# Performance work log

Measured on AMD Instinct MI355X. Metric: run time of the kernel, lower is better.

The kernel has to match this reference:

```python
import jax, jax.numpy as jnp
import numpy as np

DRUG_DIM, PROT_DIM, HIDDEN_DIM, OUTPUT_DIM = 128, 128, 256, 256


def setup_inputs() -> dict:
    key = jax.random.key(0)
    ks = jax.random.split(key, 7)
    B, n_d, n_p = 8, 64, 1024
    s = lambda d: 1.0 / np.sqrt(d)
    return {
        "X_d": jax.random.normal(ks[0], (B, n_d, DRUG_DIM), dtype=jnp.float32),
        "X_p": jax.random.normal(ks[1], (B, n_p, PROT_DIM), dtype=jnp.float32),
        # nn.Linear(in, out) weights have shape (out, in); we store transposed (in, out)
        "W_d": jax.random.uniform(ks[2], (DRUG_DIM, HIDDEN_DIM), jnp.float32, -s(DRUG_DIM), s(DRUG_DIM)),
        "W_p": jax.random.uniform(ks[3], (PROT_DIM, HIDDEN_DIM), jnp.float32, -s(PROT_DIM), s(PROT_DIM)),
        "W_a": jax.random.uniform(ks[4], (DRUG_DIM, OUTPUT_DIM), jnp.float32, -s(DRUG_DIM), s(DRUG_DIM)),
        "W_b": jax.random.uniform(ks[5], (PROT_DIM, OUTPUT_DIM), jnp.float32, -s(PROT_DIM), s(PROT_DIM)),
        "w_score": jax.random.uniform(ks[6], (HIDDEN_DIM,), jnp.float32, -s(HIDDEN_DIM), s(HIDDEN_DIM)),
    }


def reference(X_d, X_p, W_d, W_p, W_a, W_b, w_score):
    # Projections: (B, n_d, H), (B, n_p, H), (B, n_d, O), (B, n_p, O)
    hd = jnp.einsum("bik,kh->bih", X_d, W_d)
    hp = jnp.einsum("bjk,kh->bjh", X_p, W_p)
    fd = jnp.einsum("bik,ko->bio", X_d, W_a)
    fp = jnp.einsum("bjk,ko->bjo", X_p, W_b)

    # N_ij = tanh(hd_i + hp_j): (B, n_d, n_p, H); scores = N @ w_score
    N = jnp.tanh(hd[:, :, None, :] + hp[:, None, :, :])
    scores = jnp.einsum("bijh,h->bij", N, w_score)
    A = jax.nn.softmax(scores, axis=-1)  # softmax over protein dim

    # f_ij = tanh(fd_i + fp_j): (B, n_d, n_p, O)
    f = jnp.tanh(fd[:, :, None, :] + fp[:, None, :, :])
    X_int = jnp.einsum("bij,bijo->bo", A, f)  # sum over i and j
    return X_int
```

## Files before the change

kernel.cpp:

```cpp
#include <hip/hip_runtime.h>

#define NB   8
#define ND   64
#define NP   1024
#define KDIM 128
#define HID  256
#define OUTD 256
#define CSC  2.885390081777927f
#define PSTR 520

typedef __attribute__((ext_vector_type(8))) short  bf16x8;
typedef __attribute__((ext_vector_type(4))) float  f32x4;


__device__ __forceinline__ ushort f2bf(float f) {
    unsigned u = __float_as_uint(f);
    return (ushort)((u + 0x7FFFu + ((u >> 16) & 1u)) >> 16);
}

__global__ __launch_bounds__(256) void k_cast(
    const float* __restrict__ Xd, const float* __restrict__ Xp,
    const float* __restrict__ Wd, const float* __restrict__ Wa,
    const float* __restrict__ Wp, const float* __restrict__ Wb,
    ushort* __restrict__ Xdbf, ushort* __restrict__ Xpbf,
    ushort* __restrict__ WdT, ushort* __restrict__ WaT,
    ushort* __restrict__ WpT, ushort* __restrict__ WbT) {
    int blk = blockIdx.x, t = threadIdx.x;
    if (blk < 1024) {
        size_t i = ((size_t)blk << 10) + ((size_t)t << 2);
        float4 v = *(const float4*)(Xp + i);
        ushort4 o; o.x = f2bf(v.x); o.y = f2bf(v.y); o.z = f2bf(v.z); o.w = f2bf(v.w);
        *(ushort4*)(Xpbf + i) = o;
    } else if (blk < 1088) {
        size_t i = ((size_t)(blk - 1024) << 10) + ((size_t)t << 2);
        float4 v = *(const float4*)(Xd + i);
        ushort4 o; o.x = f2bf(v.x); o.y = f2bf(v.y); o.z = f2bf(v.z); o.w = f2bf(v.w);
        *(ushort4*)(Xdbf + i) = o;
    } else {
        int r = blk - 1088, mat = r >> 5;
        const float* W = (mat == 0) ? Wd : (mat == 1) ? Wa : (mat == 2) ? Wp : Wb;
        ushort* WT = (mat == 0) ? WdT : (mat == 1) ? WaT : (mat == 2) ? WpT : WbT;
        int o0 = ((r & 31) << 10) + (t << 2);
        int n = o0 >> 7, k0 = o0 & 127;
        ushort4 o;
        o.x = f2bf(W[(k0 + 0) * HID + n]);
        o.y = f2bf(W[(k0 + 1) * HID + n]);
        o.z = f2bf(W[(k0 + 2) * HID + n]);
        o.w = f2bf(W[(k0 + 3) * HID + n]);
        *(ushort4*)(WT + o0) = o;
    }
}

__global__ __launch_bounds__(256) void k_proj_mfma(
    const ushort* __restrict__ Xpbf, const ushort* __restrict__ Xdbf,
    const ushort* __restrict__ WdT, const ushort* __restrict__ WaT,
    const ushort* __restrict__ WpT, const ushort* __restrict__ WbT,
    float* __restrict__ Ehd, float* __restrict__ Efd,
    float* __restrict__ EhpT, float* __restrict__ Efp) {
    int blk = blockIdx.x, t = threadIdx.x;
    const ushort *A, *B;
    float* out; size_t obase; int ostride, am0, bn0;
    if (blk < 512) {
        int mt = blk >> 2, nt = blk & 3;
        A = Xpbf; am0 = mt * 64; B = WbT; bn0 = nt * 64;
        out = Efp; obase = (size_t)am0 * HID + bn0; ostride = HID;
    } else if (blk < 1024) {
        int r = blk - 512, b = r >> 6, rr = r & 63;
        int mt = rr >> 4, nt = rr & 15;
        A = WpT; am0 = mt * 64;
        B = Xpbf + (size_t)b * NP * KDIM; bn0 = nt * 64;
        out = EhpT; obase = ((size_t)(b * 256 + am0)) * NP + bn0; ostride = NP;
    } else if (blk < 1056) {
        int r = blk - 1024; int mt = r >> 2, nt = r & 3;
        A = Xdbf; am0 = mt * 64; B = WdT; bn0 = nt * 64;
        out = Ehd; obase = (size_t)am0 * HID + bn0; ostride = HID;
    } else {
        int r = blk - 1056; int mt = r >> 2, nt = r & 3;
        A = Xdbf; am0 = mt * 64; B = WaT; bn0 = nt * 64;
        out = Efd; obase = (size_t)am0 * HID + bn0; ostride = HID;
    }
    int l = t & 63, w = t >> 6;
    int wm = (w >> 1) << 5, wn = (w & 1) << 5;
    int lr = l & 15, lk = (l >> 4) << 3;
    const ushort* Ab = A + (size_t)(am0 + wm + lr) * KDIM + lk;
    const ushort* Bb = B + (size_t)(bn0 + wn + lr) * KDIM + lk;

    bf16x8 af[2][4], bfr[2][4];
#pragma unroll
    for (int f = 0; f < 2; ++f)
#pragma unroll
        for (int ks = 0; ks < 4; ++ks) {
            af[f][ks]  = *(const bf16x8*)(Ab + (size_t)(f << 4) * KDIM + (ks << 5));
            bfr[f][ks] = *(const bf16x8*)(Bb + (size_t)(f << 4) * KDIM + (ks << 5));
        }

    f32x4 acc[2][2];
#pragma unroll
    for (int mf = 0; mf < 2; ++mf)
#pragma unroll
        for (int nf = 0; nf < 2; ++nf) acc[mf][nf] = (f32x4){0.f, 0.f, 0.f, 0.f};
#pragma unroll
    for (int ks = 0; ks < 4; ++ks)
#pragma unroll
        for (int mf = 0; mf < 2; ++mf)
#pragma unroll
            for (int nf = 0; nf < 2; ++nf)
                acc[mf][nf] = __builtin_amdgcn_mfma_f32_16x16x32_bf16(
                    af[mf][ks], bfr[nf][ks], acc[mf][nf], 0, 0, 0);

#pragma unroll
    for (int mf = 0; mf < 2; ++mf)
#pragma unroll
        for (int nf = 0; nf < 2; ++nf)
#pragma unroll
            for (int r = 0; r < 4; ++r) {
                int m = wm + (mf << 4) + ((l >> 4) << 2) + r;
                int n = wn + (nf << 4) + (l & 15);
                out[obase + (size_t)m * ostride + n] =
                    __builtin_amdgcn_exp2f(acc[mf][nf][r] * CSC);
            }
}

__global__ __launch_bounds__(512, 8) void k_fused(
    const float* __restrict__ Ehd, const float* __restrict__ EhpT,
    const float* __restrict__ Efd, const float* __restrict__ Efp,
    const float* __restrict__ wsc, float* __restrict__ num,
    float* __restrict__ den) {
    int blk = blockIdx.x;
    int b = blk & 7, pair = (blk >> 3) & 31, jh = blk >> 8;
    int row0 = b * ND + pair * 2;
    int t = threadIdx.x;

    __shared__ float2 hrow[256];
    __shared__ float  w2s[256];
    __shared__ float2 a2[256];
    __shared__ float  sred[8 * PSTR];
    __shared__ float  wsum0[4], wsum1[4];

    if (t < 256) {
        hrow[t] = make_float2(Ehd[((size_t)row0 << 8) + t],
                              Ehd[((size_t)(row0 + 1) << 8) + t]);
        w2s[t] = -2.0f * wsc[t];
    }
    __syncthreads();

    {
        int jq = t & 63, hq = t >> 6;
        const float* pB = EhpT + ((size_t)((b << 8) + (hq << 5))) * NP
                        + (jh << 8) + (jq << 2);
        float a00 = 0, a01 = 0, a02 = 0, a03 = 0;
        float a10 = 0, a11 = 0, a12 = 0, a13 = 0;
        for (int hh = 0; hh < 32; ++hh) {
            int h = (hq << 5) + hh;
            float2 hv = hrow[h];
            float wv = w2s[h];
            float4 p = *(const float4*)(pB + (size_t)hh * NP);
            a00 = fmaf(wv, __builtin_amdgcn_rcpf(fmaf(hv.x, p.x, 1.f)), a00);
            a01 = fmaf(wv, __builtin_amdgcn_rcpf(fmaf(hv.x, p.y, 1.f)), a01);
            a02 = fmaf(wv, __builtin_amdgcn_rcpf(fmaf(hv.x, p.z, 1.f)), a02);
            a03 = fmaf(wv, __builtin_amdgcn_rcpf(fmaf(hv.x, p.w, 1.f)), a03);
            a10 = fmaf(wv, __builtin_amdgcn_rcpf(fmaf(hv.y, p.x, 1.f)), a10);
            a11 = fmaf(wv, __builtin_amdgcn_rcpf(fmaf(hv.y, p.y, 1.f)), a11);
            a12 = fmaf(wv, __builtin_amdgcn_rcpf(fmaf(hv.y, p.z, 1.f)), a12);
            a13 = fmaf(wv, __builtin_amdgcn_rcpf(fmaf(hv.y, p.w, 1.f)), a13);
        }
        int base = (hq << 6) + jq;
        sred[0 * PSTR + base] = a00;  sred[1 * PSTR + base] = a01;
        sred[2 * PSTR + base] = a02;  sred[3 * PSTR + base] = a03;
        sred[4 * PSTR + base] = a10;  sred[5 * PSTR + base] = a11;
        sred[6 * PSTR + base] = a12;  sred[7 * PSTR + base] = a13;
    }
    __syncthreads();

    if (t < 256) {
        int jq2 = t >> 2, joff = t & 3;
        const float* p0 = sred + joff * PSTR + jq2;
        const float* p1 = sred + (4 + joff) * PSTR + jq2;
        float sc0 = 0.f, sc1 = 0.f;
#pragma unroll
        for (int hq = 0; hq < 8; ++hq) {
            sc0 += p0[hq << 6];
            sc1 += p1[hq << 6];
        }
        const float L2E = 1.4426950408889634f;
        float u0 = __builtin_amdgcn_exp2f(sc0 * L2E);
        float u1 = __builtin_amdgcn_exp2f(sc1 * L2E);
        a2[t] = make_float2(-2.f * u0, -2.f * u1);
        float s0 = u0, s1 = u1;
#pragma unroll
        for (int off = 32; off > 0; off >>= 1) {
            s0 += __shfl_xor(s0, off, 64);
            s1 += __shfl_xor(s1, off, 64);
        }
        if ((t & 63) == 0) { wsum0[t >> 6] = s0; wsum1[t >> 6] = s1; }
    }
    __syncthreads();
    if (t == 0) {
        den[((size_t)row0 << 2) + jh] =
            (wsum0[0] + wsum0[1]) + (wsum0[2] + wsum0[3]);
        den[((size_t)(row0 + 1) << 2) + jh] =
            (wsum1[0] + wsum1[1]) + (wsum1[2] + wsum1[3]);
    }

    {
        int oq = t & 63, jg = t >> 6;
        int o0 = oq << 2;
        float4 fd0 = *(const float4*)(Efd + ((size_t)row0 << 8) + o0);
        float4 fd1 = *(const float4*)(Efd + ((size_t)(row0 + 1) << 8) + o0);
        const float* fpB = Efp + ((size_t)(b * NP + (jh << 8) + (jg << 5)) << 8) + o0;
        float b00 = 0, b01 = 0, b02 = 0, b03 = 0;
        float b10 = 0, b11 = 0, b12 = 0, b13 = 0;
        for (int jj = 0; jj < 32; ++jj) {
            float4 f = *(const float4*)(fpB + ((size_t)jj << 8));
            float2 av = a2[(jg << 5) + jj];
            b00 = fmaf(av.x, __builtin_amdgcn_rcpf(fmaf(fd0.x, f.x, 1.f)), b00);
            b01 = fmaf(av.x, __builtin_amdgcn_rcpf(fmaf(fd0.y, f.y, 1.f)), b01);
            b02 = fmaf(av.x, __builtin_amdgcn_rcpf(fmaf(fd0.z, f.z, 1.f)), b02);
            b03 = fmaf(av.x, __builtin_amdgcn_rcpf(fmaf(fd0.w, f.w, 1.f)), b03);
            b10 = fmaf(av.y, __builtin_amdgcn_rcpf(fmaf(fd1.x, f.x, 1.f)), b10);
            b11 = fmaf(av.y, __builtin_amdgcn_rcpf(fmaf(fd1.y, f.y, 1.f)), b11);
            b12 = fmaf(av.y, __builtin_amdgcn_rcpf(fmaf(fd1.z, f.z, 1.f)), b12);
            b13 = fmaf(av.y, __builtin_amdgcn_rcpf(fmaf(fd1.w, f.w, 1.f)), b13);
        }
        __syncthreads();
        int base = (jg << 6) + oq;
        sred[0 * PSTR + base] = b00;  sred[1 * PSTR + base] = b01;
        sred[2 * PSTR + base] = b02;  sred[3 * PSTR + base] = b03;
        sred[4 * PSTR + base] = b10;  sred[5 * PSTR + base] = b11;
        sred[6 * PSTR + base] = b12;  sred[7 * PSTR + base] = b13;
    }
    __syncthreads();

    {
        int r = t >> 8, o = t & 255;
        const float* pk = sred + ((r << 2) + (o & 3)) * PSTR + (o >> 2);
        float s = 0.f;
#pragma unroll
        for (int g = 0; g < 8; ++g) s += pk[g << 6];
        num[(((size_t)(row0 + r) << 2) + jh) * 256 + o] = s;
    }
}

__global__ __launch_bounds__(256) void k_reduce(
    const float* __restrict__ num, const float* __restrict__ den,
    float* __restrict__ out) {
    int b = blockIdx.x, t = threadIdx.x;
    float s = 64.0f;
    for (int i = 0; i < 64; ++i) {
        size_t row = (size_t)(b * 64 + i);
        float D = (den[(row << 2) + 0] + den[(row << 2) + 1]) +
                  (den[(row << 2) + 2] + den[(row << 2) + 3]);
        const float* nb = num + (row << 2) * 256 + t;
        float n = (nb[0] + nb[256]) + (nb[512] + nb[768]);
        s += n * __builtin_amdgcn_rcpf(D);
    }
    out[(b << 8) + t] = s;
}

extern "C" void kernel_launch(void* const* d_in, const int* in_sizes, int n_in,
                              void* d_out, int out_size, void* d_ws, size_t ws_size,
                              hipStream_t stream) {
    const float* Xd  = (const float*)d_in[0];
    const float* Xp  = (const float*)d_in[1];
    const float* Wd  = (const float*)d_in[2];
    const float* Wp  = (const float*)d_in[3];
    const float* Wa  = (const float*)d_in[4];
    const float* Wb  = (const float*)d_in[5];
    const float* wsc = (const float*)d_in[6];
    float* out = (float*)d_out;

    float* ws = (float*)d_ws;
    float* Ehd  = ws;
    float* Efd  = Ehd + NB * ND * HID;
    float* EhpT = Efd + NB * ND * OUTD;
    float* Efp  = EhpT + NB * NP * HID;
    float* stage = Efp + NB * NP * OUTD;
    ushort* Xpbf = (ushort*)stage;
    ushort* Xdbf = Xpbf + NB * NP * KDIM;
    ushort* WdT  = Xdbf + 65536;
    ushort* WaT  = WdT + 32768;
    ushort* WpT  = WaT + 32768;
    ushort* WbT  = WpT + 32768;
    float* numb = stage + 622592;
    float* denb = numb + 524288;

    k_cast     <<<1216, 256, 0, stream>>>(Xd, Xp, Wd, Wa, Wp, Wb,
                                          Xdbf, Xpbf, WdT, WaT, WpT, WbT);
    k_proj_mfma<<<1088, 256, 0, stream>>>(Xpbf, Xdbf, WdT, WaT, WpT, WbT,
                                          Ehd, Efd, EhpT, Efp);
    k_fused    <<<1024, 512, 0, stream>>>(Ehd, EhpT, Efd, Efp, wsc, numb, denb);
    k_reduce   <<<NB, 256, 0, stream>>>(numb, denb, out);
}
```

Baseline: 64.96 us.

## Merge four reciprocals into one and process four drug rows per block

The fused attention kernel now combines four weighted reciprocal terms, sum c_i/u_i, into a single rational expression. This needs one rcp per four terms instead of four, cutting transcendental-unit work in both the score and output loops. Each block also handles four drug rows instead of two, so every loaded protein vector is reused across more rows and the grid is halved. In exchange, register and LDS use grow (launch bounds relaxed to 4 waves per SIMD), and the product of four denominators may overflow or underflow for extreme values, which affects accuracy.

```diff
diff --git a/kernel.cpp b/kernel.cpp
--- a/kernel.cpp
+++ b/kernel.cpp
@@ -8,6 +8,7 @@
 #define OUTD 256
 #define CSC  2.885390081777927f
 #define PSTR 520
+#define AST  264
 
 typedef __attribute__((ext_vector_type(8))) short  bf16x8;
 typedef __attribute__((ext_vector_type(4))) float  f32x4;
@@ -16,6 +17,17 @@
 __device__ __forceinline__ ushort f2bf(float f) {
     unsigned u = __float_as_uint(f);
     return (ushort)((u + 0x7FFFu + ((u >> 16) & 1u)) >> 16);
+}
+
+__device__ __forceinline__ float comb4(float u1, float u2, float u3, float u4,
+                                       float c1, float c2, float c3, float c4,
+                                       float acc) {
+    float p12 = u1 * u2, p34 = u3 * u4;
+    float P   = p12 * p34;
+    float t1  = fmaf(c1, u2, c2 * u1);
+    float t2  = fmaf(c3, u4, c4 * u3);
+    float num = fmaf(t1, p34, t2 * p12);
+    return fmaf(num, __builtin_amdgcn_rcpf(P), acc);
 }
 
 __global__ __launch_bounds__(256) void k_cast(
@@ -121,25 +133,27 @@
             }
 }
 
-__global__ __launch_bounds__(512, 8) void k_fused(
+__global__ __launch_bounds__(512, 4) void k_fused(
     const float* __restrict__ Ehd, const float* __restrict__ EhpT,
     const float* __restrict__ Efd, const float* __restrict__ Efp,
     const float* __restrict__ wsc, float* __restrict__ num,
     float* __restrict__ den) {
     int blk = blockIdx.x;
-    int b = blk & 7, pair = (blk >> 3) & 31, jh = blk >> 8;
-    int row0 = b * ND + pair * 2;
+    int b = blk & 7, quad = (blk >> 3) & 15, jo = blk >> 7;
+    int row0 = b * ND + quad * 4;
     int t = threadIdx.x;
 
-    __shared__ float2 hrow[256];
+    __shared__ float4 hrow4[256];
     __shared__ float  w2s[256];
-    __shared__ float2 a2[256];
-    __shared__ float  sred[8 * PSTR];
-    __shared__ float  wsum0[4], wsum1[4];
+    __shared__ float  a2s[4 * AST];
+    __shared__ float  sred[16 * PSTR];
+    __shared__ float  wsA[8], wsB[8];
 
     if (t < 256) {
-        hrow[t] = make_float2(Ehd[((size_t)row0 << 8) + t],
-                              Ehd[((size_t)(row0 + 1) << 8) + t]);
+        hrow4[t] = make_float4(Ehd[((size_t)row0 << 8) + t],
+                               Ehd[((size_t)(row0 + 1) << 8) + t],
+                               Ehd[((size_t)(row0 + 2) << 8) + t],
+                               Ehd[((size_t)(row0 + 3) << 8) + t]);
         w2s[t] = -2.0f * wsc[t];
     }
     __syncthreads();
@@ -147,59 +161,82 @@
     {
         int jq = t & 63, hq = t >> 6;
         const float* pB = EhpT + ((size_t)((b << 8) + (hq << 5))) * NP
-                        + (jh << 8) + (jq << 2);
-        float a00 = 0, a01 = 0, a02 = 0, a03 = 0;
-        float a10 = 0, a11 = 0, a12 = 0, a13 = 0;
-        for (int hh = 0; hh < 32; ++hh) {
-            int h = (hq << 5) + hh;
-            float2 hv = hrow[h];
-            float wv = w2s[h];
-            float4 p = *(const float4*)(pB + (size_t)hh * NP);
-            a00 = fmaf(wv, __builtin_amdgcn_rcpf(fmaf(hv.x, p.x, 1.f)), a00);
-            a01 = fmaf(wv, __builtin_amdgcn_rcpf(fmaf(hv.x, p.y, 1.f)), a01);
-            a02 = fmaf(wv, __builtin_amdgcn_rcpf(fmaf(hv.x, p.z, 1.f)), a02);
-            a03 = fmaf(wv, __builtin_amdgcn_rcpf(fmaf(hv.x, p.w, 1.f)), a03);
-            a10 = fmaf(wv, __builtin_amdgcn_rcpf(fmaf(hv.y, p.x, 1.f)), a10);
-            a11 = fmaf(wv, __builtin_amdgcn_rcpf(fmaf(hv.y, p.y, 1.f)), a11);
-            a12 = fmaf(wv, __builtin_amdgcn_rcpf(fmaf(hv.y, p.z, 1.f)), a12);
-            a13 = fmaf(wv, __builtin_amdgcn_rcpf(fmaf(hv.y, p.w, 1.f)), a13);
+                        + (jo << 8) + (jq << 2);
+        float acc[4][4];
+#pragma unroll
+        for (int r = 0; r < 4; ++r)
+#pragma unroll
+            for (int c = 0; c < 4; ++c) acc[r][c] = 0.f;
+        for (int hg = 0; hg < 8; ++hg) {
+            const float* pr = pB + (size_t)(hg << 2) * NP;
+            float4 p0 = *(const float4*)(pr);
+            float4 p1 = *(const float4*)(pr + NP);
+            float4 p2 = *(const float4*)(pr + 2 * (size_t)NP);
+            float4 p3 = *(const float4*)(pr + 3 * (size_t)NP);
+            int h = (hq << 5) + (hg << 2);
+            float4 h0 = hrow4[h],     h1 = hrow4[h + 1];
+            float4 h2 = hrow4[h + 2], h3 = hrow4[h + 3];
+            float w0 = w2s[h],     w1 = w2s[h + 1];
+            float w2 = w2s[h + 2], w3 = w2s[h + 3];
+#define ROW1(HC, AR)                                                          \
+            AR[0] = comb4(fmaf(h0.HC, p0.x, 1.f), fmaf(h1.HC, p1.x, 1.f),     \
+                          fmaf(h2.HC, p2.x, 1.f), fmaf(h3.HC, p3.x, 1.f),     \
+                          w0, w1, w2, w3, AR[0]);                             \
+            AR[1] = comb4(fmaf(h0.HC, p0.y, 1.f), fmaf(h1.HC, p1.y, 1.f),     \
+                          fmaf(h2.HC, p2.y, 1.f), fmaf(h3.HC, p3.y, 1.f),     \
+                          w0, w1, w2, w3, AR[1]);                             \
+            AR[2] = comb4(fmaf(h0.HC, p0.z, 1.f), fmaf(h1.HC, p1.z, 1.f),     \
+                          fmaf(h2.HC, p2.z, 1.f), fmaf(h3.HC, p3.z, 1.f),     \
+                          w0, w1, w2, w3, AR[2]);                             \
+            AR[3] = comb4(fmaf(h0.HC, p0.w, 1.f), fmaf(h1.HC, p1.w, 1.f),     \
+                          fmaf(h2.HC, p2.w, 1.f), fmaf(h3.HC, p3.w, 1.f),     \
+                          w0, w1, w2, w3, AR[3])
+            ROW1(x, acc[0]);
+            ROW1(y, acc[1]);
+            ROW1(z, acc[2]);
+            ROW1(w, acc[3]);
+#undef ROW1
         }
         int base = (hq << 6) + jq;
-        sred[0 * PSTR + base] = a00;  sred[1 * PSTR + base] = a01;
-        sred[2 * PSTR + base] = a02;  sred[3 * PSTR + base] = a03;
-        sred[4 * PSTR + base] = a10;  sred[5 * PSTR + base] = a11;
-        sred[6 * PSTR + base] = a12;  sred[7 * PSTR + base] = a13;
+#pragma unroll
+        for (int r = 0; r < 4; ++r)
+#pragma unroll
+            for (int c = 0; c < 4; ++c)
+                sred[((r << 2) + c) * PSTR + base] = acc[r][c];
     }
     __syncthreads();
 
-    if (t < 256) {
-        int jq2 = t >> 2, joff = t & 3;
-        const float* p0 = sred + joff * PSTR + jq2;
-        const float* p1 = sred + (4 + joff) * PSTR + jq2;
-        float sc0 = 0.f, sc1 = 0.f;
+    {
+        int j = t & 255, rh = t >> 8;
+        int jq2 = j >> 2, jc = j & 3;
+        int rA = rh << 1, rB = rA + 1;
+        const float* pA = sred + ((rA << 2) + jc) * PSTR + jq2;
+        const float* pB2 = sred + ((rB << 2) + jc) * PSTR + jq2;
+        float sA = 0.f, sB = 0.f;
 #pragma unroll
         for (int hq = 0; hq < 8; ++hq) {
-            sc0 += p0[hq << 6];
-            sc1 += p1[hq << 6];
+            sA += pA[hq << 6];
+            sB += pB2[hq << 6];
         }
         const float L2E = 1.4426950408889634f;
-        float u0 = __builtin_amdgcn_exp2f(sc0 * L2E);
-        float u1 = __builtin_amdgcn_exp2f(sc1 * L2E);
-        a2[t] = make_float2(-2.f * u0, -2.f * u1);
-        float s0 = u0, s1 = u1;
+        float uA = __builtin_amdgcn_exp2f(sA * L2E);
+        float uB = __builtin_amdgcn_exp2f(sB * L2E);
+        a2s[rA * AST + j] = -2.f * uA;
+        a2s[rB * AST + j] = -2.f * uB;
+        float tA = uA, tB = uB;
 #pragma unroll
         for (int off = 32; off > 0; off >>= 1) {
-            s0 += __shfl_xor(s0, off, 64);
-            s1 += __shfl_xor(s1, off, 64);
-        }
-        if ((t & 63) == 0) { wsum0[t >> 6] = s0; wsum1[t >> 6] = s1; }
+            tA += __shfl_xor(tA, off, 64);
+            tB += __shfl_xor(tB, off, 64);
+        }
+        if ((t & 63) == 0) { wsA[t >> 6] = tA; wsB[t >> 6] = tB; }
     }
     __syncthreads();
     if (t == 0) {
-        den[((size_t)row0 << 2) + jh] =
-            (wsum0[0] + wsum0[1]) + (wsum0[2] + wsum0[3]);
-        den[((size_t)(row0 + 1) << 2) + jh] =
-            (wsum1[0] + wsum1[1]) + (wsum1[2] + wsum1[3]);
+        den[((size_t)(row0 + 0) << 2) + jo] = (wsA[0] + wsA[1]) + (wsA[2] + wsA[3]);
+        den[((size_t)(row0 + 1) << 2) + jo] = (wsB[0] + wsB[1]) + (wsB[2] + wsB[3]);
+        den[((size_t)(row0 + 2) << 2) + jo] = (wsA[4] + wsA[5]) + (wsA[6] + wsA[7]);
+        den[((size_t)(row0 + 3) << 2) + jo] = (wsB[4] + wsB[5]) + (wsB[6] + wsB[7]);
     }
 
     {
@@ -207,37 +244,63 @@
         int o0 = oq << 2;
         float4 fd0 = *(const float4*)(Efd + ((size_t)row0 << 8) + o0);
         float4 fd1 = *(const float4*)(Efd + ((size_t)(row0 + 1) << 8) + o0);
-        const float* fpB = Efp + ((size_t)(b * NP + (jh << 8) + (jg << 5)) << 8) + o0;
-        float b00 = 0, b01 = 0, b02 = 0, b03 = 0;
-        float b10 = 0, b11 = 0, b12 = 0, b13 = 0;
-        for (int jj = 0; jj < 32; ++jj) {
-            float4 f = *(const float4*)(fpB + ((size_t)jj << 8));
-            float2 av = a2[(jg << 5) + jj];
-            b00 = fmaf(av.x, __builtin_amdgcn_rcpf(fmaf(fd0.x, f.x, 1.f)), b00);
-            b01 = fmaf(av.x, __builtin_amdgcn_rcpf(fmaf(fd0.y, f.y, 1.f)), b01);
-            b02 = fmaf(av.x, __builtin_amdgcn_rcpf(fmaf(fd0.z, f.z, 1.f)), b02);
-            b03 = fmaf(av.x, __builtin_amdgcn_rcpf(fmaf(fd0.w, f.w, 1.f)), b03);
-            b10 = fmaf(av.y, __builtin_amdgcn_rcpf(fmaf(fd1.x, f.x, 1.f)), b10);
-            b11 = fmaf(av.y, __builtin_amdgcn_rcpf(fmaf(fd1.y, f.y, 1.f)), b11);
-            b12 = fmaf(av.y, __builtin_amdgcn_rcpf(fmaf(fd1.z, f.z, 1.f)), b12);
-            b13 = fmaf(av.y, __builtin_amdgcn_rcpf(fmaf(fd1.w, f.w, 1.f)), b13);
+        float4 fd2 = *(const float4*)(Efd + ((size_t)(row0 + 2) << 8) + o0);
+        float4 fd3 = *(const float4*)(Efd + ((size_t)(row0 + 3) << 8) + o0);
+        const float* fpB = Efp + ((size_t)(b * NP + (jo << 8) + (jg << 5)) << 8) + o0;
+        float bcc[4][4];
+#pragma unroll
+        for (int r = 0; r < 4; ++r)
+#pragma unroll
+            for (int c = 0; c < 4; ++c) bcc[r][c] = 0.f;
+        for (int g = 0; g < 8; ++g) {
+            const float* fr = fpB + ((size_t)(g << 2) << 8);
+            float4 f0 = *(const float4*)(fr);
+            float4 f1 = *(const float4*)(fr + 256);
+            float4 f2 = *(const float4*)(fr + 512);
+            float4 f3 = *(const float4*)(fr + 768);
+            int j0 = (jg << 5) + (g << 2);
+#define ROW3(FD, RI, BR)                                                      \
+            {                                                                 \
+                float c0 = a2s[RI * AST + j0],     c1 = a2s[RI * AST + j0 + 1];\
+                float c2 = a2s[RI * AST + j0 + 2], c3 = a2s[RI * AST + j0 + 3];\
+                BR[0] = comb4(fmaf(FD.x, f0.x, 1.f), fmaf(FD.x, f1.x, 1.f),   \
+                              fmaf(FD.x, f2.x, 1.f), fmaf(FD.x, f3.x, 1.f),   \
+                              c0, c1, c2, c3, BR[0]);                         \
+                BR[1] = comb4(fmaf(FD.y, f0.y, 1.f), fmaf(FD.y, f1.y, 1.f),   \
+                              fmaf(FD.y, f2.y, 1.f), fmaf(FD.y, f3.y, 1.f),   \
+                              c0, c1, c2, c3, BR[1]);                         \
+                BR[2] = comb4(fmaf(FD.z, f0.z, 1.f), fmaf(FD.z, f1.z, 1.f),   \
+                              fmaf(FD.z, f2.z, 1.f), fmaf(FD.z, f3.z, 1.f),   \
+                              c0, c1, c2, c3, BR[2]);                         \
+                BR[3] = comb4(fmaf(FD.w, f0.w, 1.f), fmaf(FD.w, f1.w, 1.f),   \
+                              fmaf(FD.w, f2.w, 1.f), fmaf(FD.w, f3.w, 1.f),   \
+                              c0, c1, c2, c3, BR[3]);                         \
+            }
+            ROW3(fd0, 0, bcc[0]);
+            ROW3(fd1, 1, bcc[1]);
+            ROW3(fd2, 2, bcc[2]);
+            ROW3(fd3, 3, bcc[3]);
+#undef ROW3
         }
         __syncthreads();
         int base = (jg << 6) + oq;
-        sred[0 * PSTR + base] = b00;  sred[1 * PSTR + base] = b01;
-        sred[2 * PSTR + base] = b02;  sred[3 * PSTR + base] = b03;
-        sred[4 * PSTR + base] = b10;  sred[5 * PSTR + base] = b11;
-        sred[6 * PSTR + base] = b12;  sred[7 * PSTR + base] = b13;
+#pragma unroll
+        for (int r = 0; r < 4; ++r)
+#pragma unroll
+            for (int c = 0; c < 4; ++c)
+                sred[((r << 2) + c) * PSTR + base] = bcc[r][c];
     }
     __syncthreads();
 
-    {
-        int r = t >> 8, o = t & 255;
+#pragma unroll
+    for (int rh2 = 0; rh2 < 2; ++rh2) {
+        int r = (t >> 8) + (rh2 << 1);
+        int o = t & 255;
         const float* pk = sred + ((r << 2) + (o & 3)) * PSTR + (o >> 2);
         float s = 0.f;
 #pragma unroll
         for (int g = 0; g < 8; ++g) s += pk[g << 6];
-        num[(((size_t)(row0 + r) << 2) + jh) * 256 + o] = s;
+        num[((((size_t)(row0 + r) << 2) + jo) << 8) + o] = s;
     }
 }
 
@@ -250,7 +313,7 @@
         size_t row = (size_t)(b * 64 + i);
         float D = (den[(row << 2) + 0] + den[(row << 2) + 1]) +
                   (den[(row << 2) + 2] + den[(row << 2) + 3]);
-        const float* nb = num + (row << 2) * 256 + t;
+        const float* nb = num + (row << 10) + t;
         float n = (nb[0] + nb[256]) + (nb[512] + nb[768]);
         s += n * __builtin_amdgcn_rcpf(D);
     }
@@ -281,13 +344,13 @@
     ushort* WaT  = WdT + 32768;
     ushort* WpT  = WaT + 32768;
     ushort* WbT  = WpT + 32768;
-    float* numb = stage + 622592;
-    float* denb = numb + 524288;
+    float* numb = stage;
+    float* denb = stage + 622592;
 
     k_cast     <<<1216, 256, 0, stream>>>(Xd, Xp, Wd, Wa, Wp, Wb,
                                           Xdbf, Xpbf, WdT, WaT, WpT, WbT);
     k_proj_mfma<<<1088, 256, 0, stream>>>(Xpbf, Xdbf, WdT, WaT, WpT, WbT,
                                           Ehd, Efd, EhpT, Efp);
-    k_fused    <<<1024, 512, 0, stream>>>(Ehd, EhpT, Efd, Efp, wsc, numb, denb);
+    k_fused    <<<512, 512, 0, stream>>>(Ehd, EhpT, Efd, Efp, wsc, numb, denb);
     k_reduce   <<<NB, 256, 0, stream>>>(numb, denb, out);
 }
```

Measured after the change: 62.01 us. 1.05x faster.
